# Kernel tuning notes

Hardware: AMD Instinct MI355X
Metric: run time of the kernel (lower is better)

Reference implementation:

```python
import jax, jax.numpy as jnp
import numpy as np

B, T, D, H = 2, 2048, 1024, 16
Dh = D // H


def _rope(q, k):
    # q, k: (B, H, T, Dh), interleaved even/odd rotation
    t = q.shape[2]
    dh = q.shape[3]
    inv_freq = 1.0 / (10000.0 ** (jnp.arange(0, dh, 2, dtype=jnp.float32) / dh))
    pos = jnp.arange(t, dtype=jnp.float32)
    freqs = pos[:, None] * inv_freq[None, :]          # (T, Dh/2)
    sin = jnp.sin(freqs)[None, None]                  # (1,1,T,Dh/2)
    cos = jnp.cos(freqs)[None, None]

    def rot(x):
        xe, xo = x[..., ::2], x[..., 1::2]
        re = xe * cos - xo * sin
        ro = xe * sin + xo * cos
        return jnp.stack([re, ro], axis=-1).reshape(x.shape)

    return rot(q), rot(k)


def setup_inputs() -> dict:
    key = jax.random.key(0)
    k1, k2, k3 = jax.random.split(key, 3)
    s = 1.0 / np.sqrt(D)
    return {
        "x": jax.random.normal(k1, (B, T, D), dtype=jnp.float32),
        "w_qkv": jax.random.normal(k2, (3 * D, D), dtype=jnp.float32) * s,
        "b_qkv": jnp.zeros((3 * D,), dtype=jnp.float32),
        "w_out": jax.random.normal(k3, (D, D), dtype=jnp.float32) * s,
        "b_out": jnp.zeros((D,), dtype=jnp.float32),
    }


def reference(x, w_qkv, b_qkv, w_out, b_out):
    b, t, d = x.shape
    qkv = x @ w_qkv.T + b_qkv                         # (B,T,3D)
    q, k, v = jnp.split(qkv, 3, axis=-1)
    q = q.reshape(b, t, H, Dh).transpose(0, 2, 1, 3)  # (B,H,T,Dh)
    k = k.reshape(b, t, H, Dh).transpose(0, 2, 1, 3)
    v = v.reshape(b, t, H, Dh).transpose(0, 2, 1, 3)
    q, k = _rope(q, k)
    scores = jnp.einsum("bhtd,bhsd->bhts", q, k) / jnp.sqrt(jnp.float32(Dh))
    causal = jnp.tril(jnp.ones((t, t), dtype=bool))[None, None]
    scores = jnp.where(causal, scores, -jnp.inf)
    probs = jax.nn.softmax(scores, axis=-1)
    out = jnp.einsum("bhts,bhsd->bhtd", probs, v)     # (B,H,T,Dh)
    out = out.transpose(0, 2, 1, 3).reshape(b, t, d)
    return out @ w_out.T + b_out
```

## Files before the change

### kernel.cpp

```cpp
#include <hip/hip_runtime.h>
#include <hip/hip_bf16.h>
#include <math.h>
#include <type_traits>

#define B_ 2
#define T_ 2048
#define D_ 1024
#define H_ 16
#define DH_ 64

typedef __bf16 bf16_t;
typedef bf16_t bf16x8 __attribute__((ext_vector_type(8)));
typedef bf16_t bf16x4 __attribute__((ext_vector_type(4)));
typedef float f32x4 __attribute__((ext_vector_type(4)));

typedef __attribute__((address_space(1))) const void gas_void;
typedef __attribute__((address_space(3))) void las_void;

__device__ __forceinline__ void gld16(const void* g, void* l) {
    __builtin_amdgcn_global_load_lds((gas_void*)g, (las_void*)l, 16, 0, 0);
}

#define WAITALL() asm volatile("s_waitcnt vmcnt(0) lgkmcnt(0)" ::: "memory")
#define BARRIER() do { asm volatile("" ::: "memory"); __builtin_amdgcn_s_barrier(); asm volatile("" ::: "memory"); } while (0)

__global__ __launch_bounds__(256) void cvt3(const float* __restrict__ a,
                                            const float* __restrict__ b,
                                            const float* __restrict__ c,
                                            bf16_t* __restrict__ oa,
                                            bf16_t* __restrict__ ob,
                                            bf16_t* __restrict__ oc,
                                            float2* __restrict__ tab) {
    if (blockIdx.x >= 8192) {
        int j = (blockIdx.x - 8192) * 256 + threadIdx.x;
        int t = j >> 5, d2 = j & 31;
        float invf = exp2f(-(float)d2 * 0.4152410118609203f);
        float ang = (float)t * invf;
        float sn, cs;
        sincosf(ang, &sn, &cs);
        tab[j] = make_float2(cs, sn);
        return;
    }
    int i = blockIdx.x * 256 + threadIdx.x;
    const float* src; bf16_t* dst; int off;
    if (i < 1048576)      { src = a; dst = oa; off = i; }
    else if (i < 1835008) { src = b; dst = ob; off = i - 1048576; }
    else                  { src = c; dst = oc; off = i - 1835008; }
    float4 f = ((const float4*)src)[off];
    bf16x4 v = { (bf16_t)f.x, (bf16_t)f.y, (bf16_t)f.z, (bf16_t)f.w };
    ((bf16x4*)dst)[off] = v;
}

__global__ __launch_bounds__(512, 4) void gemmqkv(const bf16_t* __restrict__ A,
                                                  const bf16_t* __restrict__ Bw,
                                                  const float* __restrict__ bias,
                                                  const float2* __restrict__ tab,
                                                  bf16_t* __restrict__ q_out,
                                                  bf16_t* __restrict__ k_out,
                                                  bf16_t* __restrict__ vt_out) {
    __shared__ __align__(16) char smem[65536];

    int tid = threadIdx.x;
    int lane = tid & 63, wid = tid >> 6;
    int wm = wid >> 2, wn = wid & 3;
    int lr = lane & 15, lk = lane >> 4;

    int l = blockIdx.y * 12 + blockIdx.x;
    int u = (l & 7) * 48 + (l >> 3);
    int bx = u % 12;
    int by = u / 12;

    f32x4 acc[4][4];
    f32x4 z = {0.f, 0.f, 0.f, 0.f};
#pragma unroll
    for (int i = 0; i < 4; i++)
#pragma unroll
        for (int j = 0; j < 4; j++) acc[i][j] = z;

    int cb = (tid & 3) * 16;
    int rT = tid >> 2;
    int sw = cb ^ (((rT >> 1) & 3) << 4);
    const char* gAp  = (const char*)A  + ((size_t)(by * 128 + rT)) * 2048 + sw;
    const char* gBp0 = (const char*)Bw + ((size_t)(bx * 256 + rT)) * 2048 + sw;
    const char* gBp1 = (const char*)Bw + ((size_t)(bx * 256 + 128 + rT)) * 2048 + sw;

    auto stg = [&](int par, int kt) __attribute__((always_inline)) {
        char* base = smem + par * 24576;
        gld16(gAp  + kt * 64, base + tid * 16);
        gld16(gBp0 + kt * 64, base + 8192 + tid * 16);
        gld16(gBp1 + kt * 64, base + 16384 + tid * 16);
    };

    int offA[4], offB[4];
#pragma unroll
    for (int m = 0; m < 4; m++) {
        int row = wm * 64 + m * 16 + lr;
        offA[m] = row * 64 + ((lk * 16) ^ (((row >> 1) & 3) << 4));
    }
#pragma unroll
    for (int n = 0; n < 4; n++) {
        int row = wn * 64 + n * 16 + lr;
        offB[n] = 8192 + row * 64 + ((lk * 16) ^ (((row >> 1) & 3) << 4));
    }

    stg(0, 0);
    for (int kt = 0; kt < 32; ++kt) {
        const char* buf = smem + (kt & 1) * 24576;
        WAITALL();
        BARRIER();
        if (kt < 31) stg((kt + 1) & 1, kt + 1);
        bf16x8 Af[4], Bf[4];
#pragma unroll
        for (int m = 0; m < 4; m++) Af[m] = *(const bf16x8*)(buf + offA[m]);
#pragma unroll
        for (int n = 0; n < 4; n++) Bf[n] = *(const bf16x8*)(buf + offB[n]);
        __builtin_amdgcn_s_setprio(1);
#pragma unroll
        for (int m = 0; m < 4; m++)
#pragma unroll
            for (int n = 0; n < 4; n++)
                acc[m][n] = __builtin_amdgcn_mfma_f32_16x16x32_bf16(Af[m], Bf[n], acc[m][n], 0, 0, 0);
        __builtin_amdgcn_s_setprio(0);
    }
    WAITALL();
    BARRIER();

    int m_base = by * 128 + wm * 64;
    int n_base = bx * 256 + wn * 64;
    char* myL = smem + wid * 8192;
    int which = n_base >> 10;
    int h = (n_base & 1023) >> 6;
    int b = m_base >> 11, t0 = m_base & 2047;
    int bh = b * H_ + h;
    if (which == 2) {
#pragma unroll
        for (int m = 0; m < 4; m++)
#pragma unroll
            for (int n = 0; n < 4; n++) {
                int rd = n * 16 + lr;
                float bv = bias[n_base + rd];
#pragma unroll
                for (int j = 0; j < 4; j++) {
                    int ct = m * 16 + lk * 4 + j;
                    int ct2 = (ct & 32) | (((ct >> 2) & 3) << 3) | (((ct >> 4) & 1) << 2) | (ct & 3);
                    int addr = (rd * 128 + ct2 * 2) ^ ((rd & 7) << 4);
                    *(bf16_t*)(myL + addr) = (bf16_t)(acc[m][n][j] + bv);
                }
            }
#pragma unroll
        for (int it = 0; it < 8; it++) {
            int row = it * 8 + (lane >> 3);
            int byt = (lane & 7) * 16;
            bf16x8 val = *(const bf16x8*)(myL + ((row * 128 + byt) ^ ((row & 7) << 4)));
            *(bf16x8*)(vt_out + ((size_t)bh * DH_ + row) * T_ + t0 + (lane & 7) * 8) = val;
        }
    } else {
        bf16_t* dst = which ? k_out : q_out;
        float qscl = which ? 1.0f : 0.18033688011112042f;
#pragma unroll
        for (int m = 0; m < 4; m++)
#pragma unroll
            for (int n = 0; n < 4; n++) {
                int dh = n * 16 + lr;
                float bv = bias[n_base + dh];
                int dh2 = dh >> 1;
                bool even = (dh & 1) == 0;
#pragma unroll
                for (int j = 0; j < 4; j++) {
                    int rt = m * 16 + lk * 4 + j;
                    float v = acc[m][n][j] + bv;
                    float pp = __shfl_xor(v, 1);
                    float2 cs = tab[(t0 + rt) * 32 + dh2];
                    float r = even ? v * cs.x - pp * cs.y : v * cs.x + pp * cs.y;
                    r *= qscl;
                    int addr = (rt * 128 + dh * 2) ^ ((rt & 7) << 4);
                    *(bf16_t*)(myL + addr) = (bf16_t)r;
                }
            }
#pragma unroll
        for (int it = 0; it < 8; it++) {
            int row = it * 8 + (lane >> 3);
            int byt = (lane & 7) * 16;
            bf16x8 val = *(const bf16x8*)(myL + ((row * 128 + byt) ^ ((row & 7) << 4)));
            *(bf16x8*)(dst + ((size_t)bh * T_ + t0 + row) * DH_ + (lane & 7) * 8) = val;
        }
    }
}

__global__ __launch_bounds__(256) void gemm128o(const bf16_t* __restrict__ A,
                                                const bf16_t* __restrict__ Bw,
                                                const float* __restrict__ bias,
                                                float* __restrict__ f_out,
                                                int K, int N) {
    __shared__ __align__(16) char smem[49152];
    char* b0 = smem;
    char* b1 = smem + 16384;
    char* b2 = smem + 32768;

    int tid = threadIdx.x;
    int lane = tid & 63, wid = tid >> 6;
    int wr = wid >> 1, wc = wid & 1;
    int lr = lane & 15, lk = lane >> 4;

    int l = blockIdx.y * gridDim.x + blockIdx.x;
    int chunk = (gridDim.x * gridDim.y) >> 3;
    int u = (l & 7) * chunk + (l >> 3);
    int bx = u % gridDim.x;
    int by = u / gridDim.x;

    f32x4 acc[4][4];
    f32x4 z = {0.f, 0.f, 0.f, 0.f};
#pragma unroll
    for (int i = 0; i < 4; i++)
#pragma unroll
        for (int j = 0; j < 4; j++) acc[i][j] = z;

    const char* Ab = (const char*)(A + (size_t)by * 128 * K);
    const char* Bb = (const char*)(Bw + (size_t)bx * 128 * K);
    const int rowstride = K * 2;

    int p0 = tid * 16;
    int p1 = 4096 + tid * 16;
    int r0 = p0 >> 6, r1 = p1 >> 6;
    int cb0 = (p0 & 63) ^ (((r0 >> 1) & 3) << 4);
    int cb1 = (p1 & 63) ^ (((r1 >> 1) & 3) << 4);
    size_t gA0 = (size_t)r0 * rowstride + cb0;
    size_t gA1 = (size_t)r1 * rowstride + cb1;

    int oa[4], ob[4];
#pragma unroll
    for (int m = 0; m < 4; m++) {
        int row = wr * 64 + m * 16 + lr;
        oa[m] = row * 64 + ((lk * 16) ^ (((row >> 1) & 3) << 4));
    }
#pragma unroll
    for (int n = 0; n < 4; n++) {
        int row = wc * 64 + n * 16 + lr;
        ob[n] = row * 64 + ((lk * 16) ^ (((row >> 1) & 3) << 4));
    }

    auto stg = [&](char* buf, int ks) __attribute__((always_inline)) {
        const char* Ag = Ab + (size_t)ks * 64;
        const char* Bg = Bb + (size_t)ks * 64;
        gld16(Ag + gA0, buf + p0);
        gld16(Ag + gA1, buf + p1);
        gld16(Bg + gA0, buf + 8192 + p0);
        gld16(Bg + gA1, buf + 8192 + p1);
    };

    auto iterf = [&](auto vmc, char* buf, int ks, bool dostage) __attribute__((always_inline)) {
        constexpr int VM = decltype(vmc)::value;
        if constexpr (VM == 8)      asm volatile("s_waitcnt vmcnt(8)" ::: "memory");
        else if constexpr (VM == 4) asm volatile("s_waitcnt vmcnt(4)" ::: "memory");
        else                        asm volatile("s_waitcnt vmcnt(0)" ::: "memory");
        __builtin_amdgcn_s_barrier();
        asm volatile("" ::: "memory");
        bf16x8 Af[4], Bf[4];
#pragma unroll
        for (int m = 0; m < 4; m++) Af[m] = *(const bf16x8*)(buf + oa[m]);
#pragma unroll
        for (int n = 0; n < 4; n++) Bf[n] = *(const bf16x8*)(buf + 8192 + ob[n]);
#pragma unroll
        for (int m = 0; m < 4; m++)
#pragma unroll
            for (int n = 0; n < 4; n++)
                acc[m][n] = __builtin_amdgcn_mfma_f32_16x16x32_bf16(Af[m], Bf[n], acc[m][n], 0, 0, 0);
        asm volatile("" ::: "memory");
        __builtin_amdgcn_s_barrier();
        asm volatile("" ::: "memory");
        if (dostage) stg(buf, ks);
    };

    std::integral_constant<int, 8> c8;
    std::integral_constant<int, 4> c4;
    std::integral_constant<int, 0> c0;

    stg(b0, 0);
    stg(b1, 1);
    stg(b2, 2);
    for (int s = 0; s < 30; s += 3) {
        iterf(c8, b0, s + 3, s + 3 < 32);
        iterf(c8, b1, s + 4, s + 4 < 32);
        iterf(c8, b2, s + 5, s + 5 < 32);
    }
    iterf(c4, b0, 0, false);
    iterf(c0, b1, 0, false);

    int m_base = by * 128 + wr * 64;
    int n_base = bx * 128 + wc * 64;
#pragma unroll
    for (int m = 0; m < 4; m++) {
        int gm0 = m_base + m * 16 + lk * 4;
#pragma unroll
        for (int n = 0; n < 4; n++) {
            int nc = n_base + n * 16 + lr;
            float bv = bias[nc];
#pragma unroll
            for (int j = 0; j < 4; j++)
                f_out[(size_t)(gm0 + j) * N + nc] = acc[m][n][j] + bv;
        }
    }
}

__global__ __launch_bounds__(256, 4) void attn128(const bf16_t* __restrict__ Q,
                                                  const bf16_t* __restrict__ K,
                                                  const bf16_t* __restrict__ Vt,
                                                  bf16_t* __restrict__ Ao) {
    __shared__ __align__(16) char smem[40960];

    int tid = threadIdx.x;
    int lane = tid & 63, wid = tid >> 6;
    int lr = lane & 15, lk = lane >> 4;
    int xcd = blockIdx.x & 7, idx = blockIdx.x >> 3;
    int bh = xcd * 4 + (idx & 3);
    int i4 = idx >> 2;
    int qt = (i4 < 8) ? i4 : 23 - i4;
    int q0 = qt * 128;
    int qrelw = wid * 16 + lr;

    const bf16_t* Qp0 = Q + ((size_t)bh * T_ + q0 + qrelw) * DH_;
    const bf16_t* Qp1 = Qp0 + 64 * DH_;
    bf16x8 qa0 = *(const bf16x8*)(Qp0 + lk * 8);
    bf16x8 qa1 = *(const bf16x8*)(Qp0 + 32 + lk * 8);
    bf16x8 qb0 = *(const bf16x8*)(Qp1 + lk * 8);
    bf16x8 qb1 = *(const bf16x8*)(Qp1 + 32 + lk * 8);

    f32x4 zz = {0.f, 0.f, 0.f, 0.f};
    f32x4 oa0[4], oa1[4];
#pragma unroll
    for (int dt = 0; dt < 4; dt++) { oa0[dt] = zz; oa1[dt] = zz; }
    float ls0 = 0.f, ls1 = 0.f;
    bf16x8 pA0, pA1, pB0, pB1;

    const char* Kbase = (const char*)(K + (size_t)bh * T_ * DH_);
    const char* Vbase = (const char*)(Vt + (size_t)bh * DH_ * T_);

    auto stage = [&](int s, char* Kd, char* Vd) __attribute__((always_inline)) {
        int kv0 = s * 64;
        const char* Kg = Kbase + (size_t)kv0 * 128;
#pragma unroll
        for (int c = 0; c < 2; c++) {
            int o = c * 4096 + tid * 16;
            int r = o >> 7;
            int g = o ^ ((r & 7) << 4);
            gld16(Kg + g, Kd + o);
            gld16(Vbase + (size_t)r * (T_ * 2) + kv0 * 2 + (g & 127), Vd + o);
        }
    };

    auto do_qk = [&](const char* Kc, int m0, int m1) __attribute__((always_inline)) {
#pragma unroll
        for (int kt = 0; kt < 4; kt++) {
            int row = kt * 16 + lr;
            int key = (row & 7) << 4;
            bf16x8 kf0 = *(const bf16x8*)(Kc + ((row * 128 + lk * 16) ^ key));
            bf16x8 kf1 = *(const bf16x8*)(Kc + ((row * 128 + 64 + lk * 16) ^ key));
            if (m0 != 2) {
                f32x4 s = zz;
                s = __builtin_amdgcn_mfma_f32_16x16x32_bf16(kf0, qa0, s, 0, 0, 0);
                s = __builtin_amdgcn_mfma_f32_16x16x32_bf16(kf1, qa1, s, 0, 0, 0);
#pragma unroll
                for (int j = 0; j < 4; j++) {
                    float sv = s[j];
                    if (m0 == 1) {
                        int kv = kt * 16 + lk * 4 + j;
                        sv = (kv <= qrelw) ? sv : -__builtin_inff();
                    }
                    float e = exp2f(sv);
                    ls0 += e;
                    if (kt < 2) pA0[kt * 4 + j] = (bf16_t)e;
                    else        pA1[(kt - 2) * 4 + j] = (bf16_t)e;
                }
            }
            {
                f32x4 s = zz;
                s = __builtin_amdgcn_mfma_f32_16x16x32_bf16(kf0, qb0, s, 0, 0, 0);
                s = __builtin_amdgcn_mfma_f32_16x16x32_bf16(kf1, qb1, s, 0, 0, 0);
#pragma unroll
                for (int j = 0; j < 4; j++) {
                    float sv = s[j];
                    if (m1 == 1) {
                        int kv = kt * 16 + lk * 4 + j;
                        sv = (kv <= qrelw) ? sv : -__builtin_inff();
                    }
                    float e = exp2f(sv);
                    ls1 += e;
                    if (kt < 2) pB0[kt * 4 + j] = (bf16_t)e;
                    else        pB1[(kt - 2) * 4 + j] = (bf16_t)e;
                }
            }
        }
    };

    auto do_pv = [&](const char* Vc, bool g0on) __attribute__((always_inline)) {
#pragma unroll
        for (int dt = 0; dt < 4; dt++) {
            int row = dt * 16 + lr;
            int key = (row & 7) << 4;
            bf16x8 vf0 = *(const bf16x8*)(Vc + ((row * 128 + lk * 16) ^ key));
            bf16x8 vf1 = *(const bf16x8*)(Vc + ((row * 128 + 64 + lk * 16) ^ key));
            if (g0on) {
                f32x4 o = oa0[dt];
                o = __builtin_amdgcn_mfma_f32_16x16x32_bf16(vf0, pA0, o, 0, 0, 0);
                o = __builtin_amdgcn_mfma_f32_16x16x32_bf16(vf1, pA1, o, 0, 0, 0);
                oa0[dt] = o;
            }
            f32x4 o = oa1[dt];
            o = __builtin_amdgcn_mfma_f32_16x16x32_bf16(vf0, pB0, o, 0, 0, 0);
            o = __builtin_amdgcn_mfma_f32_16x16x32_bf16(vf1, pB1, o, 0, 0, 0);
            oa1[dt] = o;
        }
    };

    stage(0, smem, smem + 16384);
    stage(1, smem + 8192, smem + 24576);
    asm volatile("s_waitcnt vmcnt(4)" ::: "memory");
    __builtin_amdgcn_s_barrier();
    asm volatile("" ::: "memory");
    do_qk(smem, qt == 0 ? 1 : 0, 0);

    char* Kr = smem + 8192;
    char* Kw = smem;
    char* Vr = smem + 16384;
    char* Vn = smem + 24576;
    char* Vw = smem + 32768;

    int last = 2 * qt;
    auto iterA = [&](int s, int m0, int m1) __attribute__((always_inline)) {
        WAITALL();
        __builtin_amdgcn_s_barrier();
        asm volatile("" ::: "memory");
        if (s + 2 <= last + 1) stage(s + 2, Kw, Vw);
        do_pv(Vr, true);
        do_qk(Kr, m0, m1);
        char* t;
        t = Kr; Kr = Kw; Kw = t;
        t = Vr; Vr = Vn; Vn = Vw; Vw = t;
    };

    for (int s = 0; s < last - 1; ++s) iterA(s, 0, 0);
    if (qt > 0) iterA(last - 1, 1, 0);
    iterA(last, 2, 1);
    do_pv(Vr, false);
    __syncthreads();

    ls0 += __shfl_xor(ls0, 16); ls0 += __shfl_xor(ls0, 32);
    ls1 += __shfl_xor(ls1, 16); ls1 += __shfl_xor(ls1, 32);
    float ri0 = __builtin_amdgcn_rcpf(ls0);
    float ri1 = __builtin_amdgcn_rcpf(ls1);

    char* myL = smem + wid * 2048;
    int b = bh >> 4, h = bh & 15;
#pragma unroll
    for (int dt = 0; dt < 4; dt++)
#pragma unroll
        for (int j = 0; j < 4; j++) {
            int dh = dt * 16 + lk * 4 + j;
            int addr = (lr * 128 + dh * 2) ^ ((lr & 7) << 4);
            *(bf16_t*)(myL + addr) = (bf16_t)(oa0[dt][j] * ri0);
        }
#pragma unroll
    for (int it = 0; it < 2; it++) {
        int row = it * 8 + (lane >> 3);
        int byt = (lane & 7) * 16;
        bf16x8 val = *(const bf16x8*)(myL + ((row * 128 + byt) ^ ((row & 7) << 4)));
        int t = q0 + wid * 16 + row;
        *(bf16x8*)(Ao + ((size_t)b * T_ + t) * D_ + h * DH_ + (lane & 7) * 8) = val;
    }
#pragma unroll
    for (int dt = 0; dt < 4; dt++)
#pragma unroll
        for (int j = 0; j < 4; j++) {
            int dh = dt * 16 + lk * 4 + j;
            int addr = (lr * 128 + dh * 2) ^ ((lr & 7) << 4);
            *(bf16_t*)(myL + addr) = (bf16_t)(oa1[dt][j] * ri1);
        }
#pragma unroll
    for (int it = 0; it < 2; it++) {
        int row = it * 8 + (lane >> 3);
        int byt = (lane & 7) * 16;
        bf16x8 val = *(const bf16x8*)(myL + ((row * 128 + byt) ^ ((row & 7) << 4)));
        int t = q0 + 64 + wid * 16 + row;
        *(bf16x8*)(Ao + ((size_t)b * T_ + t) * D_ + h * DH_ + (lane & 7) * 8) = val;
    }
}

extern "C" void kernel_launch(void* const* d_in, const int* in_sizes, int n_in,
                              void* d_out, int out_size, void* d_ws, size_t ws_size,
                              hipStream_t stream) {
    const float* x     = (const float*)d_in[0];
    const float* w_qkv = (const float*)d_in[1];
    const float* b_qkv = (const float*)d_in[2];
    const float* w_out = (const float*)d_in[3];
    const float* b_out = (const float*)d_in[4];
    float* out = (float*)d_out;

    char* ws = (char*)d_ws;
    bf16_t* xb    = (bf16_t*)(ws);
    bf16_t* wqkvb = (bf16_t*)(ws + 8388608);
    bf16_t* wob   = (bf16_t*)(ws + 14680064);
    bf16_t* qb    = (bf16_t*)(ws + 16777216);
    bf16_t* kb    = (bf16_t*)(ws + 25165824);
    bf16_t* vtb   = (bf16_t*)(ws + 33554432);
    bf16_t* ab    = (bf16_t*)(ws + 41943040);
    float2* tab   = (float2*)(ws + 41943040);

    cvt3<<<8448, 256, 0, stream>>>(x, w_qkv, w_out, xb, wqkvb, wob, tab);

    gemmqkv<<<dim3(12, 32), 512, 0, stream>>>(xb, wqkvb, b_qkv, tab, qb, kb, vtb);
    attn128<<<512, 256, 0, stream>>>(qb, kb, vtb, ab);
    gemm128o<<<dim3(8, 32), 256, 0, stream>>>(ab, wob, b_out, out, 1024, 1024);
}
```

Baseline: 108.7 us.

## Split long causal attention tiles across two blocks with a merge kernel

Reworks causal attention scheduling so each 512-block launch pairs a short query tile with half of a long query tile, and a second block handles the other KV half of the long tile. Unnormalized partial outputs and row sums go to workspace (reusing the xb region), and a new mergeB kernel sums them and normalizes. The aim is balanced per-block work across the causal triangle instead of uneven tile lengths. In exchange it adds an extra kernel launch, a partial-result round trip through global memory, and bf16 rounding of unnormalized partials.

```diff
diff --git a/kernel.cpp b/kernel.cpp
--- a/kernel.cpp
+++ b/kernel.cpp
@@ -8,6 +8,7 @@
 #define D_ 1024
 #define H_ 16
 #define DH_ 64
+#define PSLOT 16896
 
 typedef __bf16 bf16_t;
 typedef bf16_t bf16x8 __attribute__((ext_vector_type(8)));
@@ -302,38 +303,32 @@
     }
 }
 
-__global__ __launch_bounds__(256, 4) void attn128(const bf16_t* __restrict__ Q,
-                                                  const bf16_t* __restrict__ K,
-                                                  const bf16_t* __restrict__ Vt,
-                                                  bf16_t* __restrict__ Ao) {
-    __shared__ __align__(16) char smem[40960];
+__global__ __launch_bounds__(256, 4) void attnsplit(const bf16_t* __restrict__ Q,
+                                                    const bf16_t* __restrict__ K,
+                                                    const bf16_t* __restrict__ Vt,
+                                                    bf16_t* __restrict__ Ao,
+                                                    char* __restrict__ part) {
+    __shared__ __align__(16) char smem[49152];
 
     int tid = threadIdx.x;
     int lane = tid & 63, wid = tid >> 6;
     int lr = lane & 15, lk = lane >> 4;
-    int xcd = blockIdx.x & 7, idx = blockIdx.x >> 3;
-    int bh = xcd * 4 + (idx & 3);
-    int i4 = idx >> 2;
-    int qt = (i4 < 8) ? i4 : 23 - i4;
-    int q0 = qt * 128;
+    int pair = blockIdx.x & 255, half = blockIdx.x >> 8;
+    int xcd = pair & 7;
+    int bh = xcd * 4 + ((pair >> 3) & 3);
+    int a = pair >> 5;
+    int LB = 32 - 2 * a;
     int qrelw = wid * 16 + lr;
-
-    const bf16_t* Qp0 = Q + ((size_t)bh * T_ + q0 + qrelw) * DH_;
-    const bf16_t* Qp1 = Qp0 + 64 * DH_;
-    bf16x8 qa0 = *(const bf16x8*)(Qp0 + lk * 8);
-    bf16x8 qa1 = *(const bf16x8*)(Qp0 + 32 + lk * 8);
-    bf16x8 qb0 = *(const bf16x8*)(Qp1 + lk * 8);
-    bf16x8 qb1 = *(const bf16x8*)(Qp1 + 32 + lk * 8);
 
     f32x4 zz = {0.f, 0.f, 0.f, 0.f};
     f32x4 oa0[4], oa1[4];
-#pragma unroll
-    for (int dt = 0; dt < 4; dt++) { oa0[dt] = zz; oa1[dt] = zz; }
-    float ls0 = 0.f, ls1 = 0.f;
+    float ls0, ls1;
     bf16x8 pA0, pA1, pB0, pB1;
+    bf16x8 qa0, qa1, qb0, qb1;
 
     const char* Kbase = (const char*)(K + (size_t)bh * T_ * DH_);
     const char* Vbase = (const char*)(Vt + (size_t)bh * DH_ * T_);
+    int b_ = bh >> 4, h_ = bh & 15;
 
     auto stage = [&](int s, char* Kd, char* Vd) __attribute__((always_inline)) {
         int kv0 = s * 64;
@@ -412,77 +407,156 @@
         }
     };
 
-    stage(0, smem, smem + 16384);
-    stage(1, smem + 8192, smem + 24576);
-    asm volatile("s_waitcnt vmcnt(4)" ::: "memory");
-    __builtin_amdgcn_s_barrier();
-    asm volatile("" ::: "memory");
-    do_qk(smem, qt == 0 ? 1 : 0, 0);
-
-    char* Kr = smem + 8192;
-    char* Kw = smem;
-    char* Vr = smem + 16384;
-    char* Vn = smem + 24576;
-    char* Vw = smem + 32768;
-
-    int last = 2 * qt;
-    auto iterA = [&](int s, int m0, int m1) __attribute__((always_inline)) {
-        WAITALL();
-        __builtin_amdgcn_s_barrier();
-        asm volatile("" ::: "memory");
-        if (s + 2 <= last + 1) stage(s + 2, Kw, Vw);
-        do_pv(Vr, true);
-        do_qk(Kr, m0, m1);
-        char* t;
-        t = Kr; Kr = Kw; Kw = t;
-        t = Vr; Vr = Vn; Vn = Vw; Vw = t;
-    };
-
-    for (int s = 0; s < last - 1; ++s) iterA(s, 0, 0);
-    if (qt > 0) iterA(last - 1, 1, 0);
-    iterA(last, 2, 1);
-    do_pv(Vr, false);
-    __syncthreads();
-
-    ls0 += __shfl_xor(ls0, 16); ls0 += __shfl_xor(ls0, 32);
-    ls1 += __shfl_xor(ls1, 16); ls1 += __shfl_xor(ls1, 32);
-    float ri0 = __builtin_amdgcn_rcpf(ls0);
-    float ri1 = __builtin_amdgcn_rcpf(ls1);
-
-    char* myL = smem + wid * 2048;
+    auto run_phase = [&](int q0, int t0, int t1, int L, int emit, int slot)
+                     __attribute__((always_inline)) {
+        const bf16_t* Qp0 = Q + ((size_t)bh * T_ + q0 + qrelw) * DH_;
+        const bf16_t* Qp1 = Qp0 + 64 * DH_;
+        qa0 = *(const bf16x8*)(Qp0 + lk * 8);
+        qa1 = *(const bf16x8*)(Qp0 + 32 + lk * 8);
+        qb0 = *(const bf16x8*)(Qp1 + lk * 8);
+        qb1 = *(const bf16x8*)(Qp1 + 32 + lk * 8);
+#pragma unroll
+        for (int dt = 0; dt < 4; dt++) { oa0[dt] = zz; oa1[dt] = zz; }
+        ls0 = 0.f; ls1 = 0.f;
+
+        asm volatile("s_waitcnt lgkmcnt(0)" ::: "memory");
+        BARRIER();
+        char* Kw = smem;
+        char* Kr = smem + 8192;
+        char* Vr = smem + 16384;
+        char* Vn = smem + 24576;
+        char* Vw = smem + 32768;
+
+        stage(t0, Kw, Vr);
+        if (t0 + 1 < t1) {
+            stage(t0 + 1, Kr, Vn);
+            asm volatile("s_waitcnt vmcnt(4)" ::: "memory");
+        } else {
+            WAITALL();
+        }
+        BARRIER();
+        do_qk(Kw, (t0 == L - 2) ? 1 : 0, 0);
+
+        for (int s = t0; s < t1 - 1; ++s) {
+            WAITALL();
+            BARRIER();
+            if (s + 2 < t1) stage(s + 2, Kw, Vw);
+            do_pv(Vr, true);
+            int nm0 = (s + 1 == L - 2) ? 1 : ((s + 1 == L - 1) ? 2 : 0);
+            int nm1 = (s + 1 == L - 1) ? 1 : 0;
+            do_qk(Kr, nm0, nm1);
+            char* t = Kr; Kr = Kw; Kw = t;
+            t = Vr; Vr = Vn; Vn = Vw; Vw = t;
+        }
+        do_pv(Vr, t1 != L);
+
+        ls0 += __shfl_xor(ls0, 16); ls0 += __shfl_xor(ls0, 32);
+        ls1 += __shfl_xor(ls1, 16); ls1 += __shfl_xor(ls1, 32);
+
+        char* myL = smem + 40960 + wid * 2048;
+        if (emit == 0) {
+            float ri0 = __builtin_amdgcn_rcpf(ls0);
+            float ri1 = __builtin_amdgcn_rcpf(ls1);
+#pragma unroll
+            for (int dt = 0; dt < 4; dt++)
+#pragma unroll
+                for (int j = 0; j < 4; j++) {
+                    int dh = dt * 16 + lk * 4 + j;
+                    int addr = (lr * 128 + dh * 2) ^ ((lr & 7) << 4);
+                    *(bf16_t*)(myL + addr) = (bf16_t)(oa0[dt][j] * ri0);
+                }
+#pragma unroll
+            for (int it = 0; it < 2; it++) {
+                int row = it * 8 + (lane >> 3);
+                int byt = (lane & 7) * 16;
+                bf16x8 val = *(const bf16x8*)(myL + ((row * 128 + byt) ^ ((row & 7) << 4)));
+                int t = q0 + wid * 16 + row;
+                *(bf16x8*)(Ao + ((size_t)b_ * T_ + t) * D_ + h_ * DH_ + (lane & 7) * 8) = val;
+            }
+#pragma unroll
+            for (int dt = 0; dt < 4; dt++)
+#pragma unroll
+                for (int j = 0; j < 4; j++) {
+                    int dh = dt * 16 + lk * 4 + j;
+                    int addr = (lr * 128 + dh * 2) ^ ((lr & 7) << 4);
+                    *(bf16_t*)(myL + addr) = (bf16_t)(oa1[dt][j] * ri1);
+                }
+#pragma unroll
+            for (int it = 0; it < 2; it++) {
+                int row = it * 8 + (lane >> 3);
+                int byt = (lane & 7) * 16;
+                bf16x8 val = *(const bf16x8*)(myL + ((row * 128 + byt) ^ ((row & 7) << 4)));
+                int t = q0 + 64 + wid * 16 + row;
+                *(bf16x8*)(Ao + ((size_t)b_ * T_ + t) * D_ + h_ * DH_ + (lane & 7) * 8) = val;
+            }
+        } else {
+            char* slotO = part + (size_t)slot * PSLOT;
+            float* slotL = (float*)(slotO + 16384);
+#pragma unroll
+            for (int dt = 0; dt < 4; dt++)
+#pragma unroll
+                for (int j = 0; j < 4; j++) {
+                    int dh = dt * 16 + lk * 4 + j;
+                    int addr = (lr * 128 + dh * 2) ^ ((lr & 7) << 4);
+                    *(bf16_t*)(myL + addr) = (bf16_t)oa0[dt][j];
+                }
+#pragma unroll
+            for (int it = 0; it < 2; it++) {
+                int row = it * 8 + (lane >> 3);
+                int byt = (lane & 7) * 16;
+                bf16x8 val = *(const bf16x8*)(myL + ((row * 128 + byt) ^ ((row & 7) << 4)));
+                *(bf16x8*)(slotO + (size_t)(wid * 16 + row) * 128 + (lane & 7) * 16) = val;
+            }
+            if (lane < 16) slotL[wid * 16 + lr] = ls0;
+#pragma unroll
+            for (int dt = 0; dt < 4; dt++)
+#pragma unroll
+                for (int j = 0; j < 4; j++) {
+                    int dh = dt * 16 + lk * 4 + j;
+                    int addr = (lr * 128 + dh * 2) ^ ((lr & 7) << 4);
+                    *(bf16_t*)(myL + addr) = (bf16_t)oa1[dt][j];
+                }
+#pragma unroll
+            for (int it = 0; it < 2; it++) {
+                int row = it * 8 + (lane >> 3);
+                int byt = (lane & 7) * 16;
+                bf16x8 val = *(const bf16x8*)(myL + ((row * 128 + byt) ^ ((row & 7) << 4)));
+                *(bf16x8*)(slotO + (size_t)(64 + wid * 16 + row) * 128 + (lane & 7) * 16) = val;
+            }
+            if (lane < 16) slotL[64 + wid * 16 + lr] = ls1;
+        }
+    };
+
+    if (half == 0) {
+        run_phase(a * 128, 0, 2 * a + 2, 2 * a + 2, 0, -1);
+        run_phase((15 - a) * 128, 0, 15 - 2 * a, LB, 1, pair * 2);
+    } else {
+        run_phase((15 - a) * 128, 15 - 2 * a, LB, LB, 1, pair * 2 + 1);
+    }
+}
+
+__global__ __launch_bounds__(256) void mergeB(const char* __restrict__ part,
+                                              bf16_t* __restrict__ Ao) {
+    int pair = blockIdx.x >> 2, seg = blockIdx.x & 3;
+    int xcd = pair & 7;
+    int bh = xcd * 4 + ((pair >> 3) & 3);
+    int a = pair >> 5;
+    int q0B = (15 - a) * 128;
+    int tid = threadIdx.x;
+    int r = seg * 32 + (tid >> 3);
+    int cby = (tid & 7) * 16;
+    const char* s0 = part + (size_t)(pair * 2) * PSLOT;
+    const char* s1 = s0 + PSLOT;
+    bf16x8 p0 = *(const bf16x8*)(s0 + (size_t)r * 128 + cby);
+    bf16x8 p1 = *(const bf16x8*)(s1 + (size_t)r * 128 + cby);
+    float l = ((const float*)(s0 + 16384))[r] + ((const float*)(s1 + 16384))[r];
+    float ri = __builtin_amdgcn_rcpf(l);
+    bf16x8 o;
+#pragma unroll
+    for (int j = 0; j < 8; j++)
+        o[j] = (bf16_t)(((float)p0[j] + (float)p1[j]) * ri);
     int b = bh >> 4, h = bh & 15;
-#pragma unroll
-    for (int dt = 0; dt < 4; dt++)
-#pragma unroll
-        for (int j = 0; j < 4; j++) {
-            int dh = dt * 16 + lk * 4 + j;
-            int addr = (lr * 128 + dh * 2) ^ ((lr & 7) << 4);
-            *(bf16_t*)(myL + addr) = (bf16_t)(oa0[dt][j] * ri0);
-        }
-#pragma unroll
-    for (int it = 0; it < 2; it++) {
-        int row = it * 8 + (lane >> 3);
-        int byt = (lane & 7) * 16;
-        bf16x8 val = *(const bf16x8*)(myL + ((row * 128 + byt) ^ ((row & 7) << 4)));
-        int t = q0 + wid * 16 + row;
-        *(bf16x8*)(Ao + ((size_t)b * T_ + t) * D_ + h * DH_ + (lane & 7) * 8) = val;
-    }
-#pragma unroll
-    for (int dt = 0; dt < 4; dt++)
-#pragma unroll
-        for (int j = 0; j < 4; j++) {
-            int dh = dt * 16 + lk * 4 + j;
-            int addr = (lr * 128 + dh * 2) ^ ((lr & 7) << 4);
-            *(bf16_t*)(myL + addr) = (bf16_t)(oa1[dt][j] * ri1);
-        }
-#pragma unroll
-    for (int it = 0; it < 2; it++) {
-        int row = it * 8 + (lane >> 3);
-        int byt = (lane & 7) * 16;
-        bf16x8 val = *(const bf16x8*)(myL + ((row * 128 + byt) ^ ((row & 7) << 4)));
-        int t = q0 + 64 + wid * 16 + row;
-        *(bf16x8*)(Ao + ((size_t)b * T_ + t) * D_ + h * DH_ + (lane & 7) * 8) = val;
-    }
+    *(bf16x8*)(Ao + ((size_t)b * T_ + q0B + r) * D_ + h * DH_ + (cby >> 1)) = o;
 }
 
 extern "C" void kernel_launch(void* const* d_in, const int* in_sizes, int n_in,
@@ -504,10 +578,12 @@
     bf16_t* vtb   = (bf16_t*)(ws + 33554432);
     bf16_t* ab    = (bf16_t*)(ws + 41943040);
     float2* tab   = (float2*)(ws + 41943040);
+    char* partials = ws;
 
     cvt3<<<8448, 256, 0, stream>>>(x, w_qkv, w_out, xb, wqkvb, wob, tab);
 
     gemmqkv<<<dim3(12, 32), 512, 0, stream>>>(xb, wqkvb, b_qkv, tab, qb, kb, vtb);
-    attn128<<<512, 256, 0, stream>>>(qb, kb, vtb, ab);
+    attnsplit<<<512, 256, 0, stream>>>(qb, kb, vtb, ab, partials);
+    mergeB<<<1024, 256, 0, stream>>>(partials, ab);
     gemm128o<<<dim3(8, 32), 256, 0, stream>>>(ab, wob, b_out, out, 1024, 1024);
 }
```

Result: no change. 108.5 us (-0.2%).
